# Kernel optimization log

Hardware: AMD Instinct MI355X
Metric: run time of the kernel (lower is better)

## Reference

```python
import jax, jax.numpy as jnp
import numpy as np

CD_COEFF = 1.0  # init_kwargs cd_coeff

def _chamfer(p1, p2):
    # p1: (B, N, 3), p2: (B, M, 3)
    # pairwise squared distances (B, N, M)
    d2 = jnp.sum((p1[:, :, None, :] - p2[:, None, :, :]) ** 2, axis=-1)
    d = jnp.sqrt(d2)  # L2 norm as in torch.norm(dist, 2, dim=3)
    min_nm = jnp.min(d, axis=2)  # (B, N): for each pred point, nearest target
    min_mn = jnp.min(d, axis=1)  # (B, M): for each target point, nearest pred
    # batch-normalized symmetric chamfer distance
    return jnp.mean(jnp.mean(min_nm, axis=1) + jnp.mean(min_mn, axis=1))

def setup_inputs() -> dict:
    key = jax.random.key(0)
    k1, k2 = jax.random.split(key)
    x_diff_pred = jax.random.normal(k1, (8, 4096, 3), dtype=jnp.float32)
    x_diff_target = jax.random.normal(k2, (8, 4096, 3), dtype=jnp.float32)
    return {"x_diff_pred": x_diff_pred, "x_diff_target": x_diff_target}

def reference(x_diff_pred, x_diff_target):
    cd = _chamfer(x_diff_pred, x_diff_target)
    loss = CD_COEFF * cd
    return loss
```

## Files before the change

kernel.cpp:

```cpp
#include <hip/hip_runtime.h>


typedef _Float16 f16x4 __attribute__((ext_vector_type(4)));
typedef _Float16 f16x8 __attribute__((ext_vector_type(8)));
typedef float    f32x16 __attribute__((ext_vector_type(16)));

#define BATCH 8
#define NPTS 4096
#define THREADS 512
#define WAVES 8
#define HALF_PTS 2048
#define HALF_TILES (HALF_PTS/32)
#define K1_BLOCKS 256

__device__ __forceinline__ float min3f(float a, float b, float c) {
    return fminf(fminf(a, b), c);
}

__global__ __launch_bounds__(THREADS, 8) void cd_mfma(
        const float* __restrict__ pred,
        const float* __restrict__ targ,
        float* __restrict__ Bsum) {
    __shared__ uint4 sdb[HALF_PTS];
    __shared__ float wred[WAVES];
    const int bx   = blockIdx.x;
    const int tid  = threadIdx.x;
    const int dirb = bx >> 4;
    const int ctg  = bx & 15;
    const int wave = tid >> 6;
    const int lane = tid & 63;
    const int dir  = dirb >> 3;
    const int b    = dirb & 7;
    const float* Qraw = (dir ? targ : pred) + (size_t)b * NPTS * 3;
    const float* Draw = (dir ? pred : targ) + (size_t)b * NPTS * 3;

    const int q = (ctg * WAVES + wave) * 32 + (lane & 31);
    const float* qp = Qraw + (size_t)q * 3;
    _Float16 qhx = (_Float16)qp[0], qhy = (_Float16)qp[1], qhz = (_Float16)qp[2];
    float xr = (float)qhx, yr = (float)qhy, zr = (float)qhz;
    float nq = fmaf(xr, xr, fmaf(yr, yr, zr * zr));
    _Float16 mx = (_Float16)(-2.f * xr), my = (_Float16)(-2.f * yr),
             mz = (_Float16)(-2.f * zr), one = (_Float16)1.f, zz = (_Float16)0.f;
    f16x4 Bf = (lane < 32) ? (f16x4){mx, my, mz, one}
                           : (f16x4){one, zz, zz, zz};

    const f32x16 Z = {};
    const float inf = __uint_as_float(0x7F800000u);
    float m = inf;
    auto fold = [&](const f32x16& a) {
        float s0 = min3f(a[0],  a[1],  a[2]);
        float s1 = min3f(a[3],  a[4],  a[5]);
        float s2 = min3f(a[6],  a[7],  a[8]);
        float s3 = min3f(a[9],  a[10], a[11]);
        float s4 = min3f(a[12], a[13], a[14]);
        float t0 = min3f(s0, s1, s2);
        float t1 = min3f(s3, s4, a[15]);
        m = min3f(m, t0, t1);
    };

    const char* sb = (const char*)sdb;
    const int off0 = (lane & 31) * 16 + ((lane >> 5) << 3);

    #pragma unroll 1
    for (int h = 0; h < 2; ++h) {
        if (h) __syncthreads();

        for (int i = tid; i < HALF_PTS; i += THREADS) {
            const float* p = Draw + (size_t)(h * HALF_PTS + i) * 3;
            _Float16 hx = (_Float16)p[0], hy = (_Float16)p[1], hz = (_Float16)p[2];
            float xf = (float)hx, yf = (float)hy, zf = (float)hz;
            float w  = fmaf(xf, xf, fmaf(yf, yf, zf * zf));
            _Float16 hhi = (_Float16)w;
            _Float16 hlo = (_Float16)(w - (float)hhi);
            f16x8 pkt = {hx, hy, hz, hhi, hlo,
                         (_Float16)0.f, (_Float16)0.f, (_Float16)0.f};
            sdb[i] = __builtin_bit_cast(uint4, pkt);
        }
        __syncthreads();

        int off = off0;
        auto rd = [&]() { f16x4 v = *(const f16x4*)(sb + off); off += 512; return v; };
        f32x16 acc0 = __builtin_amdgcn_mfma_f32_32x32x8f16(rd(), Bf, Z, 0, 0, 0);
        f32x16 acc1 = __builtin_amdgcn_mfma_f32_32x32x8f16(rd(), Bf, Z, 0, 0, 0);
        #pragma unroll 4
        for (int j = 2; j < HALF_TILES; j += 2) {
            fold(acc0);
            acc0 = __builtin_amdgcn_mfma_f32_32x32x8f16(rd(), Bf, Z, 0, 0, 0);
            fold(acc1);
            acc1 = __builtin_amdgcn_mfma_f32_32x32x8f16(rd(), Bf, Z, 0, 0, 0);
        }
        fold(acc0);
        fold(acc1);
        __syncthreads();
    }

    m = fminf(m, __shfl_xor(m, 32, 64));
    float d = sqrtf(fmaxf(m + nq, 0.f));
    d += __shfl_xor(d, 16, 64);
    d += __shfl_xor(d,  8, 64);
    d += __shfl_xor(d,  4, 64);
    d += __shfl_xor(d,  2, 64);
    d += __shfl_xor(d,  1, 64);
    if (lane == 0) wred[wave] = d;
    __syncthreads();
    if (tid == 0) {
        float s = ((wred[0] + wred[1]) + (wred[2] + wred[3]))
                + ((wred[4] + wred[5]) + (wred[6] + wred[7]));
        Bsum[bx] = s;
    }
}

__global__ __launch_bounds__(256) void cd_final(
        const float* __restrict__ Bsum, float* __restrict__ out) {
    const int tid = threadIdx.x;
    float s = Bsum[tid];
    __shared__ float red[256];
    red[tid] = s;
    __syncthreads();
    for (int off = 128; off > 0; off >>= 1) {
        if (tid < off) red[tid] += red[tid + off];
        __syncthreads();
    }
    if (tid == 0) out[0] = red[0] * (1.0f / (float)(BATCH * NPTS));
}

extern "C" void kernel_launch(void* const* d_in, const int* in_sizes, int n_in,
                              void* d_out, int out_size, void* d_ws, size_t ws_size,
                              hipStream_t stream) {
    const float* pred = (const float*)d_in[0];
    const float* targ = (const float*)d_in[1];
    float* Bsum = (float*)d_ws;
    float* out  = (float*)d_out;

    cd_mfma<<<K1_BLOCKS, THREADS, 0, stream>>>(pred, targ, Bsum);
    cd_final<<<1, 256, 0, stream>>>(Bsum, out);
}
```

Measured before the change: 15.81 us.

## Split database across wave pairs and double block count for more parallelism

Each block now stages all 4096 database points into LDS at once, removing the two-phase load and its extra barriers. Each block covers 128 query points instead of 256, and two groups of four waves each scan half of the database. Per-query minima are combined through shared memory before the sqrt and sum. This doubles the grid to 512 blocks so more work runs in parallel, at the cost of 64KB of LDS per block and each block re-staging the full database.

```diff
diff --git a/kernel.cpp b/kernel.cpp
--- a/kernel.cpp
+++ b/kernel.cpp
@@ -8,25 +8,24 @@
 #define BATCH 8
 #define NPTS 4096
 #define THREADS 512
-#define WAVES 8
-#define HALF_PTS 2048
-#define HALF_TILES (HALF_PTS/32)
-#define K1_BLOCKS 256
+#define K1_BLOCKS 512
+#define HALF_TILES 64
 
 __device__ __forceinline__ float min3f(float a, float b, float c) {
     return fminf(fminf(a, b), c);
 }
 
-__global__ __launch_bounds__(THREADS, 8) void cd_mfma(
+__global__ __launch_bounds__(THREADS, 4) void cd_mfma(
         const float* __restrict__ pred,
         const float* __restrict__ targ,
         float* __restrict__ Bsum) {
-    __shared__ uint4 sdb[HALF_PTS];
-    __shared__ float wred[WAVES];
+    __shared__ uint4 sdb[NPTS];
+    __shared__ float wpart[8][32];
+    __shared__ float wred[4];
     const int bx   = blockIdx.x;
     const int tid  = threadIdx.x;
-    const int dirb = bx >> 4;
-    const int ctg  = bx & 15;
+    const int dirb = bx >> 5;
+    const int ctg  = bx & 31;
     const int wave = tid >> 6;
     const int lane = tid & 63;
     const int dir  = dirb >> 3;
@@ -34,7 +33,8 @@
     const float* Qraw = (dir ? targ : pred) + (size_t)b * NPTS * 3;
     const float* Draw = (dir ? pred : targ) + (size_t)b * NPTS * 3;
 
-    const int q = (ctg * WAVES + wave) * 32 + (lane & 31);
+    const int coltile = ctg * 4 + (wave & 3);
+    const int q = coltile * 32 + (lane & 31);
     const float* qp = Qraw + (size_t)q * 3;
     _Float16 qhx = (_Float16)qp[0], qhy = (_Float16)qp[1], qhz = (_Float16)qp[2];
     float xr = (float)qhx, yr = (float)qhy, zr = (float)qhz;
@@ -43,6 +43,23 @@
              mz = (_Float16)(-2.f * zr), one = (_Float16)1.f, zz = (_Float16)0.f;
     f16x4 Bf = (lane < 32) ? (f16x4){mx, my, mz, one}
                            : (f16x4){one, zz, zz, zz};
+
+    for (int i = tid; i < NPTS; i += THREADS) {
+        const float* p = Draw + (size_t)i * 3;
+        _Float16 hx = (_Float16)p[0], hy = (_Float16)p[1], hz = (_Float16)p[2];
+        float xf = (float)hx, yf = (float)hy, zf = (float)hz;
+        float w  = fmaf(xf, xf, fmaf(yf, yf, zf * zf));
+        _Float16 hhi = (_Float16)w;
+        _Float16 hlo = (_Float16)(w - (float)hhi);
+        f16x8 pkt = {hx, hy, hz, hhi, hlo,
+                     (_Float16)0.f, (_Float16)0.f, (_Float16)0.f};
+        sdb[i] = __builtin_bit_cast(uint4, pkt);
+    }
+    __syncthreads();
+
+    const char* sb = (const char*)sdb;
+    int off = (wave >> 2) * (HALF_TILES * 512)
+            + (lane & 31) * 16 + ((lane >> 5) << 3);
 
     const f32x16 Z = {};
     const float inf = __uint_as_float(0x7F800000u);
@@ -57,63 +74,42 @@
         float t1 = min3f(s3, s4, a[15]);
         m = min3f(m, t0, t1);
     };
+    auto rd = [&]() { f16x4 v = *(const f16x4*)(sb + off); off += 512; return v; };
 
-    const char* sb = (const char*)sdb;
-    const int off0 = (lane & 31) * 16 + ((lane >> 5) << 3);
-
-    #pragma unroll 1
-    for (int h = 0; h < 2; ++h) {
-        if (h) __syncthreads();
-
-        for (int i = tid; i < HALF_PTS; i += THREADS) {
-            const float* p = Draw + (size_t)(h * HALF_PTS + i) * 3;
-            _Float16 hx = (_Float16)p[0], hy = (_Float16)p[1], hz = (_Float16)p[2];
-            float xf = (float)hx, yf = (float)hy, zf = (float)hz;
-            float w  = fmaf(xf, xf, fmaf(yf, yf, zf * zf));
-            _Float16 hhi = (_Float16)w;
-            _Float16 hlo = (_Float16)(w - (float)hhi);
-            f16x8 pkt = {hx, hy, hz, hhi, hlo,
-                         (_Float16)0.f, (_Float16)0.f, (_Float16)0.f};
-            sdb[i] = __builtin_bit_cast(uint4, pkt);
-        }
-        __syncthreads();
-
-        int off = off0;
-        auto rd = [&]() { f16x4 v = *(const f16x4*)(sb + off); off += 512; return v; };
-        f32x16 acc0 = __builtin_amdgcn_mfma_f32_32x32x8f16(rd(), Bf, Z, 0, 0, 0);
-        f32x16 acc1 = __builtin_amdgcn_mfma_f32_32x32x8f16(rd(), Bf, Z, 0, 0, 0);
-        #pragma unroll 4
-        for (int j = 2; j < HALF_TILES; j += 2) {
-            fold(acc0);
-            acc0 = __builtin_amdgcn_mfma_f32_32x32x8f16(rd(), Bf, Z, 0, 0, 0);
-            fold(acc1);
-            acc1 = __builtin_amdgcn_mfma_f32_32x32x8f16(rd(), Bf, Z, 0, 0, 0);
-        }
+    f32x16 acc0 = __builtin_amdgcn_mfma_f32_32x32x8f16(rd(), Bf, Z, 0, 0, 0);
+    f32x16 acc1 = __builtin_amdgcn_mfma_f32_32x32x8f16(rd(), Bf, Z, 0, 0, 0);
+    #pragma unroll 4
+    for (int j = 2; j < HALF_TILES; j += 2) {
         fold(acc0);
+        acc0 = __builtin_amdgcn_mfma_f32_32x32x8f16(rd(), Bf, Z, 0, 0, 0);
         fold(acc1);
-        __syncthreads();
+        acc1 = __builtin_amdgcn_mfma_f32_32x32x8f16(rd(), Bf, Z, 0, 0, 0);
     }
+    fold(acc0);
+    fold(acc1);
 
     m = fminf(m, __shfl_xor(m, 32, 64));
-    float d = sqrtf(fmaxf(m + nq, 0.f));
-    d += __shfl_xor(d, 16, 64);
-    d += __shfl_xor(d,  8, 64);
-    d += __shfl_xor(d,  4, 64);
-    d += __shfl_xor(d,  2, 64);
-    d += __shfl_xor(d,  1, 64);
-    if (lane == 0) wred[wave] = d;
+    if (lane < 32) wpart[wave][lane] = m;
     __syncthreads();
-    if (tid == 0) {
-        float s = ((wred[0] + wred[1]) + (wred[2] + wred[3]))
-                + ((wred[4] + wred[5]) + (wred[6] + wred[7]));
-        Bsum[bx] = s;
+    if (wave < 4) {
+        float m2 = fminf(wpart[wave][lane & 31], wpart[wave + 4][lane & 31]);
+        float d = sqrtf(fmaxf(m2 + nq, 0.f));
+        d += __shfl_xor(d, 16, 64);
+        d += __shfl_xor(d,  8, 64);
+        d += __shfl_xor(d,  4, 64);
+        d += __shfl_xor(d,  2, 64);
+        d += __shfl_xor(d,  1, 64);
+        if (lane == 0) wred[wave] = d;
     }
+    __syncthreads();
+    if (tid == 0)
+        Bsum[bx] = (wred[0] + wred[1]) + (wred[2] + wred[3]);
 }
 
 __global__ __launch_bounds__(256) void cd_final(
         const float* __restrict__ Bsum, float* __restrict__ out) {
     const int tid = threadIdx.x;
-    float s = Bsum[tid];
+    float s = Bsum[tid] + Bsum[tid + 256];
     __shared__ float red[256];
     red[tid] = s;
     __syncthreads();
```

New measurement: 16.13 us. 2.1% more time.

## Split database halves across blocks, reuse A tiles over two query tiles, add reduction kernel

Applied to the files above, without the earlier changes.

Each block now handles one half of the database points and 64 queries per wave instead of 32, so each A tile read from LDS feeds two MFMAs. The LDS layout changes to split 64-bit rows so that reads are contiguous per lane. Partial minima from the two halves are written to global memory and merged by a new reduction kernel that applies sqrt and sums. The cost is a third kernel launch, a global round trip for 64K partial values, and lower occupancy from launch bounds of 4.

```diff
diff --git a/kernel.cpp b/kernel.cpp
--- a/kernel.cpp
+++ b/kernel.cpp
@@ -2,31 +2,31 @@
 
 
 typedef _Float16 f16x4 __attribute__((ext_vector_type(4)));
-typedef _Float16 f16x8 __attribute__((ext_vector_type(8)));
 typedef float    f32x16 __attribute__((ext_vector_type(16)));
 
 #define BATCH 8
 #define NPTS 4096
 #define THREADS 512
-#define WAVES 8
 #define HALF_PTS 2048
-#define HALF_TILES (HALF_PTS/32)
+#define HALF_TILES 64
+#define NSLOT 65536
 #define K1_BLOCKS 256
+#define RBLKS 256
 
 __device__ __forceinline__ float min3f(float a, float b, float c) {
     return fminf(fminf(a, b), c);
 }
 
-__global__ __launch_bounds__(THREADS, 8) void cd_mfma(
+__global__ __launch_bounds__(THREADS, 4) void cd_mfma(
         const float* __restrict__ pred,
         const float* __restrict__ targ,
-        float* __restrict__ Bsum) {
-    __shared__ uint4 sdb[HALF_PTS];
-    __shared__ float wred[WAVES];
+        float* __restrict__ P) {
+    __shared__ unsigned long long sdb[HALF_PTS * 2];
     const int bx   = blockIdx.x;
     const int tid  = threadIdx.x;
     const int dirb = bx >> 4;
-    const int ctg  = bx & 15;
+    const int qg   = (bx >> 1) & 7;
+    const int h    = bx & 1;
     const int wave = tid >> 6;
     const int lane = tid & 63;
     const int dir  = dirb >> 3;
@@ -34,20 +34,43 @@
     const float* Qraw = (dir ? targ : pred) + (size_t)b * NPTS * 3;
     const float* Draw = (dir ? pred : targ) + (size_t)b * NPTS * 3;
 
-    const int q = (ctg * WAVES + wave) * 32 + (lane & 31);
-    const float* qp = Qraw + (size_t)q * 3;
-    _Float16 qhx = (_Float16)qp[0], qhy = (_Float16)qp[1], qhz = (_Float16)qp[2];
-    float xr = (float)qhx, yr = (float)qhy, zr = (float)qhz;
-    float nq = fmaf(xr, xr, fmaf(yr, yr, zr * zr));
-    _Float16 mx = (_Float16)(-2.f * xr), my = (_Float16)(-2.f * yr),
-             mz = (_Float16)(-2.f * zr), one = (_Float16)1.f, zz = (_Float16)0.f;
-    f16x4 Bf = (lane < 32) ? (f16x4){mx, my, mz, one}
+    for (int i = tid; i < HALF_PTS; i += THREADS) {
+        const float* p = Draw + (size_t)(h * HALF_PTS + i) * 3;
+        _Float16 hx = (_Float16)p[0], hy = (_Float16)p[1], hz = (_Float16)p[2];
+        float xf = (float)hx, yf = (float)hy, zf = (float)hz;
+        float w  = fmaf(xf, xf, fmaf(yf, yf, zf * zf));
+        _Float16 hhi = (_Float16)w;
+        _Float16 hlo = (_Float16)(w - (float)hhi);
+        f16x4 lo4 = {hx, hy, hz, hhi};
+        f16x4 hi4 = {hlo, (_Float16)0.f, (_Float16)0.f, (_Float16)0.f};
+        const int t = i >> 5, r = i & 31;
+        sdb[t * 64 + r]      = __builtin_bit_cast(unsigned long long, lo4);
+        sdb[t * 64 + 32 + r] = __builtin_bit_cast(unsigned long long, hi4);
+    }
+
+    const int q0 = qg * 512 + wave * 64 + (lane & 31);
+    const int q1 = q0 + 32;
+    float nq0, nq1;
+    auto mkB = [&](int q, float& nq) -> f16x4 {
+        const float* qp = Qraw + (size_t)q * 3;
+        _Float16 qx = (_Float16)qp[0], qy = (_Float16)qp[1], qz = (_Float16)qp[2];
+        float xr = (float)qx, yr = (float)qy, zr = (float)qz;
+        nq = fmaf(xr, xr, fmaf(yr, yr, zr * zr));
+        _Float16 mx = (_Float16)(-2.f * xr), my = (_Float16)(-2.f * yr),
+                 mz = (_Float16)(-2.f * zr), one = (_Float16)1.f,
+                 zz = (_Float16)0.f;
+        return (lane < 32) ? (f16x4){mx, my, mz, one}
                            : (f16x4){one, zz, zz, zz};
+    };
+    f16x4 B0 = mkB(q0, nq0);
+    f16x4 B1 = mkB(q1, nq1);
+
+    __syncthreads();
 
     const f32x16 Z = {};
     const float inf = __uint_as_float(0x7F800000u);
-    float m = inf;
-    auto fold = [&](const f32x16& a) {
+    float m0 = inf, m1 = inf;
+    auto fold = [&](const f32x16& a, float& m) {
         float s0 = min3f(a[0],  a[1],  a[2]);
         float s1 = min3f(a[3],  a[4],  a[5]);
         float s2 = min3f(a[6],  a[7],  a[8]);
@@ -58,56 +81,55 @@
         m = min3f(m, t0, t1);
     };
 
-    const char* sb = (const char*)sdb;
-    const int off0 = (lane & 31) * 16 + ((lane >> 5) << 3);
+    int idx = lane;
+    auto rdA = [&]() {
+        f16x4 v = __builtin_bit_cast(f16x4, sdb[idx]);
+        idx += 64;
+        return v;
+    };
 
-    #pragma unroll 1
-    for (int h = 0; h < 2; ++h) {
-        if (h) __syncthreads();
+    f16x4 A0 = rdA();
+    f32x16 a00 = __builtin_amdgcn_mfma_f32_32x32x8f16(A0, B0, Z, 0, 0, 0);
+    f32x16 a01 = __builtin_amdgcn_mfma_f32_32x32x8f16(A0, B1, Z, 0, 0, 0);
+    f16x4 A1 = rdA();
+    f32x16 a10 = __builtin_amdgcn_mfma_f32_32x32x8f16(A1, B0, Z, 0, 0, 0);
+    f32x16 a11 = __builtin_amdgcn_mfma_f32_32x32x8f16(A1, B1, Z, 0, 0, 0);
+    #pragma unroll 4
+    for (int j = 2; j < HALF_TILES; j += 2) {
+        f16x4 An = rdA();
+        fold(a00, m0); fold(a01, m1);
+        a00 = __builtin_amdgcn_mfma_f32_32x32x8f16(An, B0, Z, 0, 0, 0);
+        a01 = __builtin_amdgcn_mfma_f32_32x32x8f16(An, B1, Z, 0, 0, 0);
+        f16x4 Am = rdA();
+        fold(a10, m0); fold(a11, m1);
+        a10 = __builtin_amdgcn_mfma_f32_32x32x8f16(Am, B0, Z, 0, 0, 0);
+        a11 = __builtin_amdgcn_mfma_f32_32x32x8f16(Am, B1, Z, 0, 0, 0);
+    }
+    fold(a00, m0); fold(a01, m1);
+    fold(a10, m0); fold(a11, m1);
 
-        for (int i = tid; i < HALF_PTS; i += THREADS) {
-            const float* p = Draw + (size_t)(h * HALF_PTS + i) * 3;
-            _Float16 hx = (_Float16)p[0], hy = (_Float16)p[1], hz = (_Float16)p[2];
-            float xf = (float)hx, yf = (float)hy, zf = (float)hz;
-            float w  = fmaf(xf, xf, fmaf(yf, yf, zf * zf));
-            _Float16 hhi = (_Float16)w;
-            _Float16 hlo = (_Float16)(w - (float)hhi);
-            f16x8 pkt = {hx, hy, hz, hhi, hlo,
-                         (_Float16)0.f, (_Float16)0.f, (_Float16)0.f};
-            sdb[i] = __builtin_bit_cast(uint4, pkt);
-        }
-        __syncthreads();
+    m0 = fminf(m0, __shfl_xor(m0, 32, 64));
+    m1 = fminf(m1, __shfl_xor(m1, 32, 64));
+    if (lane < 32) {
+        float* Ph = P + (size_t)h * NSLOT + (size_t)dirb * NPTS;
+        Ph[q0] = m0 + nq0;
+        Ph[q1] = m1 + nq1;
+    }
+}
 
-        int off = off0;
-        auto rd = [&]() { f16x4 v = *(const f16x4*)(sb + off); off += 512; return v; };
-        f32x16 acc0 = __builtin_amdgcn_mfma_f32_32x32x8f16(rd(), Bf, Z, 0, 0, 0);
-        f32x16 acc1 = __builtin_amdgcn_mfma_f32_32x32x8f16(rd(), Bf, Z, 0, 0, 0);
-        #pragma unroll 4
-        for (int j = 2; j < HALF_TILES; j += 2) {
-            fold(acc0);
-            acc0 = __builtin_amdgcn_mfma_f32_32x32x8f16(rd(), Bf, Z, 0, 0, 0);
-            fold(acc1);
-            acc1 = __builtin_amdgcn_mfma_f32_32x32x8f16(rd(), Bf, Z, 0, 0, 0);
-        }
-        fold(acc0);
-        fold(acc1);
-        __syncthreads();
-    }
-
-    m = fminf(m, __shfl_xor(m, 32, 64));
-    float d = sqrtf(fmaxf(m + nq, 0.f));
-    d += __shfl_xor(d, 16, 64);
-    d += __shfl_xor(d,  8, 64);
-    d += __shfl_xor(d,  4, 64);
-    d += __shfl_xor(d,  2, 64);
-    d += __shfl_xor(d,  1, 64);
-    if (lane == 0) wred[wave] = d;
+__global__ __launch_bounds__(256) void cd_red(
+        const float* __restrict__ P, float* __restrict__ Bsum) {
+    const int tid  = threadIdx.x;
+    const int slot = blockIdx.x * 256 + tid;
+    float v = fminf(P[slot], P[NSLOT + slot]);
+    float d = sqrtf(fmaxf(v, 0.f));
+    #pragma unroll
+    for (int off = 32; off > 0; off >>= 1) d += __shfl_down(d, off);
+    __shared__ float wsum[4];
+    if ((tid & 63) == 0) wsum[tid >> 6] = d;
     __syncthreads();
-    if (tid == 0) {
-        float s = ((wred[0] + wred[1]) + (wred[2] + wred[3]))
-                + ((wred[4] + wred[5]) + (wred[6] + wred[7]));
-        Bsum[bx] = s;
-    }
+    if (tid == 0)
+        Bsum[blockIdx.x] = (wsum[0] + wsum[1]) + (wsum[2] + wsum[3]);
 }
 
 __global__ __launch_bounds__(256) void cd_final(
@@ -129,9 +151,11 @@
                               hipStream_t stream) {
     const float* pred = (const float*)d_in[0];
     const float* targ = (const float*)d_in[1];
-    float* Bsum = (float*)d_ws;
+    float* P    = (float*)d_ws;
+    float* Bsum = (float*)((char*)d_ws + 2 * NSLOT * 4);
     float* out  = (float*)d_out;
 
-    cd_mfma<<<K1_BLOCKS, THREADS, 0, stream>>>(pred, targ, Bsum);
+    cd_mfma<<<K1_BLOCKS, THREADS, 0, stream>>>(pred, targ, P);
+    cd_red<<<RBLKS, 256, 0, stream>>>(P, Bsum);
     cd_final<<<1, 256, 0, stream>>>(Bsum, out);
 }
```

Measured after the change: 16.27 us. 1.03x slower.
